# Optimization experiments

Hardware: AMD Instinct MI355X
Metric: run time of the kernel (lower is better)

## Reference

```python
import jax, jax.numpy as jnp
import numpy as np

N = 4096     # batch of positions
E = 32       # descriptor buckets (experts)
NBLK = 12    # residual blocks per head


def _ln(x, g, b, eps=1e-5):
    m = x.mean(-1, keepdims=True)
    v = ((x - m) ** 2).mean(-1, keepdims=True)
    return (x - m) / jnp.sqrt(v + eps) * g + b


def _gelu(x):
    return jax.nn.gelu(x, approximate=False)  # torch nn.GELU default = exact erf


def setup_inputs() -> dict:
    key = jax.random.key(0)
    ks = iter(jax.random.split(key, 64))

    def nrm(shape, scale=0.05):
        return jax.random.normal(next(ks), shape, jnp.float32) * scale

    return {
        "piece_idx": jax.random.randint(next(ks), (N, 64), 0, 12),
        "side_flag": jax.random.randint(next(ks), (N,), 0, 2),
        "ep_file": jax.random.randint(next(ks), (N,), 0, 8),
        "castle_ms": jax.random.uniform(next(ks), (N, 4), jnp.float32),
        "fifty_a": jax.random.uniform(next(ks), (N,), jnp.float32),
        "descriptor_index": jax.random.randint(next(ks), (N,), 0, E),
        # per-bucket embedding tables, stacked on a leading expert axis
        "Wp_w": nrm((E, 64, 12, 32)), "Wp_b": nrm((E, 64, 12, 32)),
        "Wc_w": nrm((E, 4, 32)), "Wc_b": nrm((E, 4, 32)),
        "Wep_w": nrm((E, 8, 32)), "Wep_b": nrm((E, 8, 32)),
        "Wf_w": nrm((E, 2, 32)), "Wf_b": nrm((E, 2, 32)),
        # per-bucket MLP head params (weights stored as [in,out])
        "fc1_w": nrm((E, 2240, 256)), "fc1_b": nrm((E, 256)),
        "ln1_g": jnp.ones((E, 256)), "ln1_b": jnp.zeros((E, 256)),
        "fc2_w": nrm((E, 256, 32)), "fc2_b": nrm((E, 32)),
        "ln2_g": jnp.ones((E, 32)), "ln2_b": jnp.zeros((E, 32)),
        "blkA_w": nrm((NBLK, E, 32, 32)), "blkA_b": nrm((NBLK, E, 32)),
        "blkA_g": jnp.ones((NBLK, E, 32)), "blkA_be": jnp.zeros((NBLK, E, 32)),
        "blkB_w": nrm((NBLK, E, 32, 32)), "blkB_b": nrm((NBLK, E, 32)),
        "blkB_g": jnp.ones((NBLK, E, 32)), "blkB_be": jnp.zeros((NBLK, E, 32)),
        "out_w": nrm((E, 32, 51)), "out_b": nrm((E, 51)),
        "bins": jnp.linspace(0.0, 1.0, 51),
    }


def reference(piece_idx, side_flag, ep_file, castle_ms, fifty_a, descriptor_index,
              Wp_w, Wp_b, Wc_w, Wc_b, Wep_w, Wep_b, Wf_w, Wf_b,
              fc1_w, fc1_b, ln1_g, ln1_b, fc2_w, fc2_b, ln2_g, ln2_b,
              blkA_w, blkA_b, blkA_g, blkA_be, blkB_w, blkB_b, blkB_g, blkB_be,
              out_w, out_b, bins):
    desc = descriptor_index
    side = side_flag.astype(bool)
    n = piece_idx.shape[0]

    # ---- per-bucket, side-selected embedding gathers -> x_emb [N,2240] ----
    sq = jnp.arange(64)
    pc = jnp.maximum(piece_idx, 0)                                 # clamp -1 -> 0
    w_emb = Wp_w[desc[:, None], sq[None, :], pc]                    # [N,64,32]
    b_emb = Wp_b[desc[:, None], sq[None, :], pc]
    piece_emb = jnp.where(side[:, None, None], b_emb, w_emb)
    piece_emb = piece_emb * (piece_idx >= 0)[..., None].astype(piece_emb.dtype)
    pieces_vec = piece_emb.reshape(n, 2048)

    Wc = jnp.where(side[:, None, None], Wc_b[desc], Wc_w[desc])     # [N,4,32]
    castle_vec = (castle_ms[..., None] * Wc).reshape(n, 128)

    Wep = jnp.where(side[:, None, None], Wep_b[desc], Wep_w[desc])  # [N,8,32]
    epc = jnp.maximum(ep_file, 0)
    ep_vec = jnp.take_along_axis(Wep, epc[:, None, None], axis=1)[:, 0]
    ep_vec = ep_vec * (ep_file >= 0)[:, None].astype(ep_vec.dtype)

    Wf = jnp.where(side[:, None, None], Wf_b[desc], Wf_w[desc])     # [N,2,32]
    fifty_vec = (1.0 - fifty_a)[:, None] * Wf[:, 0] + fifty_a[:, None] * Wf[:, 1]

    x = jnp.concatenate([pieces_vec, castle_vec, ep_vec, fifty_vec], axis=1)  # [N,2240]

    # ---- expert-routed dense layer: all-expert GEMM + per-token select ----
    def dense_moe(h, W, b):
        ha = jnp.einsum('nd,edh->neh', h, W)                        # [N,E,out]
        hsel = jnp.take_along_axis(ha, desc[:, None, None], axis=1)[:, 0]
        return hsel + b[desc]

    h = _ln(_gelu(dense_moe(x, fc1_w, fc1_b)), ln1_g[desc], ln1_b[desc])   # [N,256]
    h = _ln(_gelu(dense_moe(h, fc2_w, fc2_b)), ln2_g[desc], ln2_b[desc])   # [N,32]

    def blk(carry, p):
        wA, bA, gA, beA, wB, bB, gB, beB = p
        y = _ln(_gelu(dense_moe(carry, wA, bA)), gA[desc], beA[desc])
        y = _ln(_gelu(dense_moe(y, wB, bB)), gB[desc], beB[desc])
        return carry + y, None

    h, _ = jax.lax.scan(blk, h, (blkA_w, blkA_b, blkA_g, blkA_be,
                                 blkB_w, blkB_b, blkB_g, blkB_be))

    logits = dense_moe(_gelu(h), out_w, out_b)                      # [N,51]
    p_win = jnp.sum(jax.nn.softmax(logits, axis=-1) * bins, axis=-1, keepdims=True)
    return logits, p_win
```

## Files before the change

### kernel.cpp

```cpp
#include <hip/hip_runtime.h>
#include <math.h>

#define N 4096
#define E 32
#define NBLK 12
#define D_IN 2240
#define H1 256
#define H2 32
#define NOUT 51
#define MT 16
#define NPAD (N + E*(MT-1))
#define NTILE (NPAD/MT)
#define KSTEPS (D_IN/32)
#define KSPLIT 4
#define NROWS 4608
#define GMAX 96

typedef short s8v __attribute__((ext_vector_type(8)));
typedef float f4v __attribute__((ext_vector_type(4)));

__device__ __forceinline__ float gelu(float x){
    return 0.5f * x * (1.0f + erff(x * 0.70710678118654752f));
}
__device__ __forceinline__ unsigned short f2bf(float f){
    unsigned int u = __float_as_uint(f);
    unsigned int r = (u + 0x7fffu + ((u >> 16) & 1u)) >> 16;
    return (unsigned short)r;
}

__global__ void k_sort(const int* __restrict__ desc,
                       int* __restrict__ perm, int* __restrict__ tile_e,
                       int4* __restrict__ garr, int* __restrict__ ngroups){
    __shared__ int scnt[E];
    __shared__ int spoff[E+1];
    __shared__ int scur[E];
    int tid = threadIdx.x;
    if (tid < E) scnt[tid] = 0;
    __syncthreads();
    for (int n = tid; n < N; n += blockDim.x) atomicAdd(&scnt[desc[n]], 1);
    __syncthreads();
    if (tid == 0){
        int run = 0;
        for (int e = 0; e < E; e++){ spoff[e] = run; run += ((scnt[e] + MT - 1)/MT)*MT; }
        spoff[E] = run;
        int ng = 0;
        for (int e = 0; e < E; e++){
            int t0 = spoff[e]/MT, t1 = spoff[e+1]/MT;
            for (int t = t0; t < t1; t += 8){
                int nv = t1 - t; if (nv > 8) nv = 8;
                if (ng < GMAX) garr[ng] = make_int4(t, e, nv, 0);
                ng++;
            }
        }
        *ngroups = (ng > GMAX) ? GMAX : ng;
    }
    __syncthreads();
    if (tid < E) scur[tid] = spoff[tid];
    for (int p = tid; p < NPAD; p += blockDim.x) perm[p] = -1;
    __syncthreads();
    for (int n = tid; n < N; n += blockDim.x){
        int p = atomicAdd(&scur[desc[n]], 1);
        perm[p] = n;
    }
    for (int t = tid; t < NTILE; t += blockDim.x){
        int p0 = t*MT;
        int e = -1;
        if (p0 < spoff[E]){
            for (int q = 0; q < E; q++){
                if (p0 >= spoff[q] && p0 < spoff[q+1]){ e = q; break; }
            }
        }
        tile_e[t] = e;
    }
}

__global__ void k_convert(const float* __restrict__ W1, unsigned short* __restrict__ Wt){
    int kt = blockIdx.x;
    int nt = blockIdx.y;
    int e  = blockIdx.z;
    __shared__ float lds[64][65];
    int t = threadIdx.x;
    int k0 = kt*64, n0 = nt*64;
    int kk = t >> 4, nn = (t & 15) * 4;
    const float* src = W1 + ((size_t)e*D_IN + k0)*H1 + n0;
    #pragma unroll
    for (int r = 0; r < 4; r++){
        float4 v = *(const float4*)(src + (size_t)(kk + r*16)*H1 + nn);
        lds[kk + r*16][nn]   = v.x;
        lds[kk + r*16][nn+1] = v.y;
        lds[kk + r*16][nn+2] = v.z;
        lds[kk + r*16][nn+3] = v.w;
    }
    __syncthreads();
    int n = t >> 2, kq = t & 3;
    s8v p0, p1;
    #pragma unroll
    for (int j = 0; j < 8; j++) p0[j] = (short)f2bf(lds[kq*16 + j][n]);
    #pragma unroll
    for (int j = 0; j < 8; j++) p1[j] = (short)f2bf(lds[kq*16 + 8 + j][n]);
    unsigned short* dst = Wt + ((size_t)(e*H1 + n0 + n))*D_IN + k0 + kq*16;
    *(s8v*)dst       = p0;
    *(s8v*)(dst + 8) = p1;
}

__global__ void k_build(const int* __restrict__ perm,
                        const int* __restrict__ piece_idx,
                        const int* __restrict__ side_flag,
                        const int* __restrict__ ep_file,
                        const float* __restrict__ castle_ms,
                        const float* __restrict__ fifty_a,
                        const int* __restrict__ desc_idx,
                        const float* __restrict__ Wp_w, const float* __restrict__ Wp_b,
                        const float* __restrict__ Wc_w, const float* __restrict__ Wc_b,
                        const float* __restrict__ Wep_w, const float* __restrict__ Wep_b,
                        const float* __restrict__ Wf_w, const float* __restrict__ Wf_b,
                        unsigned short* __restrict__ xs){
    int pos = blockIdx.x;
    int row = perm[pos];
    unsigned short* xr = xs + (size_t)pos * D_IN;
    int tid = threadIdx.x;
    if (row < 0){
        s8v z = {0,0,0,0,0,0,0,0};
        for (int t = tid; t < D_IN/8; t += blockDim.x) *(s8v*)(xr + t*8) = z;
        return;
    }
    int d = desc_idx[row];
    int s = side_flag[row];
    __shared__ int pidx[64];
    if (tid < 64) pidx[tid] = piece_idx[row*64 + tid];
    __syncthreads();
    const float* Wp  = s ? Wp_b  : Wp_w;
    const float* Wc  = s ? Wc_b  : Wc_w;
    const float* Wep = s ? Wep_b : Wep_w;
    const float* Wf  = s ? Wf_b  : Wf_w;
    int ep  = ep_file[row];
    int epc = ep > 0 ? ep : 0;
    float a = fifty_a[row];
    for (int t = tid; t < D_IN/8; t += blockDim.x){
        int i0 = t*8;
        float v[8];
        if (i0 < 2048){
            int sq = i0 >> 5, c0 = i0 & 31;
            int pc = pidx[sq];
            float msk = pc >= 0 ? 1.0f : 0.0f;
            int pcc = pc > 0 ? pc : 0;
            const float* base = Wp + (((size_t)d*64 + sq)*12 + pcc)*32 + c0;
            float4 a0 = *(const float4*)base;
            float4 a1 = *(const float4*)(base + 4);
            v[0]=a0.x*msk; v[1]=a0.y*msk; v[2]=a0.z*msk; v[3]=a0.w*msk;
            v[4]=a1.x*msk; v[5]=a1.y*msk; v[6]=a1.z*msk; v[7]=a1.w*msk;
        } else if (i0 < 2176){
            int j = i0 - 2048; int ci = j >> 5, c0 = j & 31;
            float cv = castle_ms[row*4 + ci];
            const float* base = Wc + ((size_t)d*4 + ci)*32 + c0;
            float4 a0 = *(const float4*)base;
            float4 a1 = *(const float4*)(base + 4);
            v[0]=a0.x*cv; v[1]=a0.y*cv; v[2]=a0.z*cv; v[3]=a0.w*cv;
            v[4]=a1.x*cv; v[5]=a1.y*cv; v[6]=a1.z*cv; v[7]=a1.w*cv;
        } else if (i0 < 2208){
            int c0 = i0 - 2176;
            float msk = ep >= 0 ? 1.0f : 0.0f;
            const float* base = Wep + ((size_t)d*8 + epc)*32 + c0;
            float4 a0 = *(const float4*)base;
            float4 a1 = *(const float4*)(base + 4);
            v[0]=a0.x*msk; v[1]=a0.y*msk; v[2]=a0.z*msk; v[3]=a0.w*msk;
            v[4]=a1.x*msk; v[5]=a1.y*msk; v[6]=a1.z*msk; v[7]=a1.w*msk;
        } else {
            int c0 = i0 - 2208;
            #pragma unroll
            for (int j = 0; j < 8; j++)
                v[j] = (1.0f - a) * Wf[(size_t)d*64 + c0 + j] + a * Wf[(size_t)d*64 + 32 + c0 + j];
        }
        s8v p;
        #pragma unroll
        for (int j = 0; j < 8; j++) p[j] = (short)f2bf(v[j]);
        *(s8v*)(xr + i0) = p;
    }
}

__launch_bounds__(256)
__global__ void k_fc1(const int4* __restrict__ garr, const int* __restrict__ ngroups,
                      const unsigned short* __restrict__ xs,
                      const unsigned short* __restrict__ Wt,
                      float* __restrict__ h1p){
    int g = blockIdx.x;
    if (g >= *ngroups) return;
    int4 gi = garr[g];
    int tile0 = gi.x, e = gi.y, nv = gi.z;
    int kc = blockIdx.y, nh = blockIdx.z;
    int kstart = (kc <= 2) ? kc*18 : 53;
    int nsteps = (kc < 2) ? 18 : 17;
    int lane = threadIdx.x & 63, wave = threadIdx.x >> 6;
    int quad = lane >> 4, l16 = lane & 15;
    int col0 = nh*128 + wave*32 + l16;
    const unsigned short* Ab = xs + (size_t)(tile0*MT + l16)*D_IN + quad*8;
    const unsigned short* B0 = Wt + ((size_t)e*H1 + col0)*D_IN + quad*8;
    const unsigned short* B1 = B0 + (size_t)16*D_IN;
    f4v acc[8][2];
    #pragma unroll
    for (int mt = 0; mt < 8; mt++){ acc[mt][0] = (f4v){0.f,0.f,0.f,0.f}; acc[mt][1] = (f4v){0.f,0.f,0.f,0.f}; }
    int kend = kstart + nsteps;
    #pragma unroll 2
    for (int s = kstart; s < kend; s++){
        int ko = s*32;
        s8v b0 = *(const s8v*)(B0 + ko);
        s8v b1 = *(const s8v*)(B1 + ko);
        #pragma unroll
        for (int mt = 0; mt < 8; mt++){
            s8v av = *(const s8v*)(Ab + (size_t)mt*MT*D_IN + ko);
            acc[mt][0] = __builtin_amdgcn_mfma_f32_16x16x32_bf16(av, b0, acc[mt][0], 0, 0, 0);
            acc[mt][1] = __builtin_amdgcn_mfma_f32_16x16x32_bf16(av, b1, acc[mt][1], 0, 0, 0);
        }
    }
    float* out = h1p + (size_t)kc*NROWS*H1;
    #pragma unroll
    for (int mt = 0; mt < 8; mt++){
        if (mt >= nv) break;
        int posb = (tile0 + mt)*MT + quad*4;
        #pragma unroll
        for (int r = 0; r < 4; r++){
            out[(size_t)(posb + r)*H1 + col0]      = acc[mt][0][r];
            out[(size_t)(posb + r)*H1 + col0 + 16] = acc[mt][1][r];
        }
    }
}

__launch_bounds__(512)
__global__ void k_fc2(const int* __restrict__ tile_e,
                      const float* __restrict__ h1p,
                      const float* __restrict__ b1,
                      const float* __restrict__ g1, const float* __restrict__ be1,
                      const float* __restrict__ W2, const float* __restrict__ b2,
                      const float* __restrict__ g2, const float* __restrict__ be2,
                      float* __restrict__ h){
    int t = blockIdx.x;
    int e = tile_e[t];
    if (e < 0) return;
    __shared__ float sh[MT][H1+1];
    __shared__ float sW[H1*H2];
    __shared__ float sg[H1], sb[H1];
    int tid = threadIdx.x;
    const float4* Wsrc = (const float4*)(W2 + (size_t)e*H1*H2);
    for (int i = tid; i < H1*H2/4; i += 512) ((float4*)sW)[i] = Wsrc[i];
    if (tid < H1){ sg[tid] = g1[e*H1 + tid]; sb[tid] = be1[e*H1 + tid]; }
    for (int slot = tid; slot < MT*H1/4; slot += 512){
        int r = slot >> 6, c4 = (slot & 63) << 2;
        float4 sacc = {0.f,0.f,0.f,0.f};
        #pragma unroll
        for (int kc = 0; kc < KSPLIT; kc++){
            float4 v = *(const float4*)(h1p + ((size_t)kc*NROWS + t*MT + r)*H1 + c4);
            sacc.x += v.x; sacc.y += v.y; sacc.z += v.z; sacc.w += v.w;
        }
        float4 bb = *(const float4*)(b1 + e*H1 + c4);
        sh[r][c4]   = gelu(sacc.x + bb.x);
        sh[r][c4+1] = gelu(sacc.y + bb.y);
        sh[r][c4+2] = gelu(sacc.z + bb.z);
        sh[r][c4+3] = gelu(sacc.w + bb.w);
    }
    __syncthreads();
    int m = tid >> 5, c = tid & 31;
    float s = 0.f;
    for (int k = c; k < H1; k += 32) s += sh[m][k];
    for (int o = 16; o > 0; o >>= 1) s += __shfl_xor(s, o);
    float mean = s * (1.0f/H1);
    float v2 = 0.f;
    for (int k = c; k < H1; k += 32){ float d = sh[m][k] - mean; v2 += d*d; }
    for (int o = 16; o > 0; o >>= 1) v2 += __shfl_xor(v2, o);
    float rs = rsqrtf(v2 * (1.0f/H1) + 1e-5f);
    for (int k = c; k < H1; k += 32)
        sh[m][k] = (sh[m][k] - mean) * rs * sg[k] + sb[k];
    __syncthreads();
    float acc = b2[e*H2 + c];
    #pragma unroll 8
    for (int k = 0; k < H1; k++) acc = fmaf(sh[m][k], sW[k*H2 + c], acc);
    float y = gelu(acc);
    float ss = y;
    for (int o = 16; o > 0; o >>= 1) ss += __shfl_xor(ss, o);
    float mean2 = ss * (1.0f/H2);
    float dv = y - mean2;
    float vv = dv*dv;
    for (int o = 16; o > 0; o >>= 1) vv += __shfl_xor(vv, o);
    float var2 = vv * (1.0f/H2);
    float outv = dv * rsqrtf(var2 + 1e-5f) * g2[e*H2+c] + be2[e*H2+c];
    h[(size_t)(t*MT + m)*H2 + c] = outv;
}

__launch_bounds__(512)
__global__ void k_blocks(const int* __restrict__ tile_e,
                         const float* __restrict__ Aw, const float* __restrict__ Ab,
                         const float* __restrict__ Ag, const float* __restrict__ Abe,
                         const float* __restrict__ Bw, const float* __restrict__ Bb,
                         const float* __restrict__ Bg, const float* __restrict__ Bbe,
                         float* __restrict__ h){
    int t = blockIdx.x;
    int e = tile_e[t];
    if (e < 0) return;
    int m = threadIdx.x >> 5, c = threadIdx.x & 31;
    int pos = t*MT + m;
    float hv = h[(size_t)pos*H2 + c];
    __shared__ float sA[1024], sB[1024], shh[MT][33];
    for (int tb = 0; tb < NBLK; tb++){
        const float* A = Aw + ((size_t)tb*E + e)*1024;
        const float* B = Bw + ((size_t)tb*E + e)*1024;
        __syncthreads();
        for (int i = threadIdx.x; i < 1024; i += 512){ sA[i] = A[i]; sB[i] = B[i]; }
        shh[m][c] = hv;
        __syncthreads();
        float acc = Ab[((size_t)tb*E + e)*32 + c];
        #pragma unroll
        for (int k = 0; k < 32; k++) acc = fmaf(shh[m][k], sA[k*32 + c], acc);
        float y = gelu(acc);
        float s = y;
        for (int o = 16; o > 0; o >>= 1) s += __shfl_xor(s, o);
        float mean = s * (1.0f/32);
        float dv = y - mean;
        float v = dv*dv;
        for (int o = 16; o > 0; o >>= 1) v += __shfl_xor(v, o);
        float var = v * (1.0f/32);
        y = dv * rsqrtf(var + 1e-5f) * Ag[((size_t)tb*E+e)*32+c] + Abe[((size_t)tb*E+e)*32+c];
        __syncthreads();
        shh[m][c] = y;
        __syncthreads();
        acc = Bb[((size_t)tb*E + e)*32 + c];
        #pragma unroll
        for (int k = 0; k < 32; k++) acc = fmaf(shh[m][k], sB[k*32 + c], acc);
        y = gelu(acc);
        s = y;
        for (int o = 16; o > 0; o >>= 1) s += __shfl_xor(s, o);
        mean = s * (1.0f/32);
        dv = y - mean;
        v = dv*dv;
        for (int o = 16; o > 0; o >>= 1) v += __shfl_xor(v, o);
        var = v * (1.0f/32);
        y = dv * rsqrtf(var + 1e-5f) * Bg[((size_t)tb*E+e)*32+c] + Bbe[((size_t)tb*E+e)*32+c];
        hv += y;
    }
    h[(size_t)pos*H2 + c] = hv;
}

__global__ void k_out(const int* __restrict__ perm, const int* __restrict__ tile_e,
                      const float* __restrict__ h,
                      const float* __restrict__ Ow, const float* __restrict__ Ob,
                      const float* __restrict__ bins,
                      float* __restrict__ out){
    int wid = threadIdx.x >> 6, lane = threadIdx.x & 63;
    int pos = blockIdx.x*4 + wid;
    if (pos >= NPAD) return;
    int row = perm[pos];
    if (row < 0) return;
    int e = tile_e[pos / MT];
    float gv = 0.0f;
    if (lane < 32) gv = gelu(h[(size_t)pos*H2 + lane]);
    float acc = (lane < NOUT) ? Ob[e*NOUT + lane] : -INFINITY;
    const float* W = Ow + (size_t)e*32*NOUT;
    #pragma unroll
    for (int k = 0; k < 32; k++){
        float gk = __shfl(gv, k);
        if (lane < NOUT) acc = fmaf(gk, W[k*NOUT + lane], acc);
    }
    if (lane < NOUT) out[(size_t)row*NOUT + lane] = acc;
    float mx = acc;
    for (int o = 32; o > 0; o >>= 1) mx = fmaxf(mx, __shfl_xor(mx, o));
    float p = (lane < NOUT) ? expf(acc - mx) : 0.0f;
    float sum = p;
    for (int o = 32; o > 0; o >>= 1) sum += __shfl_xor(sum, o);
    float pb = (lane < NOUT) ? p * bins[lane] : 0.0f;
    float sb = pb;
    for (int o = 32; o > 0; o >>= 1) sb += __shfl_xor(sb, o);
    if (lane == 0) out[(size_t)N*NOUT + row] = sb / sum;
}

extern "C" void kernel_launch(void* const* d_in, const int* in_sizes, int n_in,
                              void* d_out, int out_size, void* d_ws, size_t ws_size,
                              hipStream_t stream){
    const int*   piece_idx = (const int*)d_in[0];
    const int*   side_flag = (const int*)d_in[1];
    const int*   ep_file   = (const int*)d_in[2];
    const float* castle_ms = (const float*)d_in[3];
    const float* fifty_a   = (const float*)d_in[4];
    const int*   desc      = (const int*)d_in[5];
    const float* Wp_w  = (const float*)d_in[6];
    const float* Wp_b  = (const float*)d_in[7];
    const float* Wc_w  = (const float*)d_in[8];
    const float* Wc_b  = (const float*)d_in[9];
    const float* Wep_w = (const float*)d_in[10];
    const float* Wep_b = (const float*)d_in[11];
    const float* Wf_w  = (const float*)d_in[12];
    const float* Wf_b  = (const float*)d_in[13];
    const float* fc1_w = (const float*)d_in[14];
    const float* fc1_b = (const float*)d_in[15];
    const float* ln1_g = (const float*)d_in[16];
    const float* ln1_b = (const float*)d_in[17];
    const float* fc2_w = (const float*)d_in[18];
    const float* fc2_b = (const float*)d_in[19];
    const float* ln2_g = (const float*)d_in[20];
    const float* ln2_b = (const float*)d_in[21];
    const float* blkA_w  = (const float*)d_in[22];
    const float* blkA_b  = (const float*)d_in[23];
    const float* blkA_g  = (const float*)d_in[24];
    const float* blkA_be = (const float*)d_in[25];
    const float* blkB_w  = (const float*)d_in[26];
    const float* blkB_b  = (const float*)d_in[27];
    const float* blkB_g  = (const float*)d_in[28];
    const float* blkB_be = (const float*)d_in[29];
    const float* out_w = (const float*)d_in[30];
    const float* out_b = (const float*)d_in[31];
    const float* bins  = (const float*)d_in[32];

    char* wsp = (char*)d_ws;
    auto alloc = [&](size_t bytes){ void* p = (void*)wsp; wsp += (bytes + 255) & ~(size_t)255; return p; };
    int*            perm    = (int*)            alloc((size_t)NPAD*4);
    int*            tile_e  = (int*)            alloc((size_t)NTILE*4);
    int4*           garr    = (int4*)           alloc((size_t)GMAX*16);
    int*            ngroups = (int*)            alloc(256);
    unsigned short* Wt      = (unsigned short*) alloc((size_t)E*H1*D_IN*2);
    unsigned short* xs      = (unsigned short*) alloc((size_t)(NPAD+128)*D_IN*2);
    float*          h1p     = (float*)          alloc((size_t)KSPLIT*NROWS*H1*4);
    float*          h       = (float*)          alloc((size_t)NPAD*H2*4);

    k_sort<<<1, 256, 0, stream>>>(desc, perm, tile_e, garr, ngroups);
    k_convert<<<dim3(D_IN/64, H1/64, E), 256, 0, stream>>>(fc1_w, Wt);
    k_build<<<NPAD, 256, 0, stream>>>(perm, piece_idx, side_flag, ep_file, castle_ms,
                                      fifty_a, desc, Wp_w, Wp_b, Wc_w, Wc_b,
                                      Wep_w, Wep_b, Wf_w, Wf_b, xs);
    k_fc1<<<dim3(GMAX, KSPLIT, 2), 256, 0, stream>>>(garr, ngroups, xs, Wt, h1p);
    k_fc2<<<NTILE, 512, 0, stream>>>(tile_e, h1p, fc1_b, ln1_g, ln1_b,
                                     fc2_w, fc2_b, ln2_g, ln2_b, h);
    k_blocks<<<NTILE, 512, 0, stream>>>(tile_e, blkA_w, blkA_b, blkA_g, blkA_be,
                                        blkB_w, blkB_b, blkB_g, blkB_be, h);
    k_out<<<(NPAD + 3)/4, 256, 0, stream>>>(perm, tile_e, h, out_w, out_b, bins, (float*)d_out);
}
```

Baseline: 330.4 us.

## Fuse fc2, residual blocks and output head into one wave-per-row tail kernel

Merges the fc2+LN, twelve residual blocks, and output/softmax kernels into a single kernel with one 64-lane wave per token row and 1024 threads per tile. The residual blocks now use wave shuffles and read weights directly from global memory instead of staging them in shared memory with block-wide barriers. The intermediate h buffer round-trip and two kernel launches go away. In exchange, each row's weight reads hit global/L2 repeatedly and the large 1024-thread blocks may reduce occupancy.

Result: slower. 374.9 us (+13.5%).

```diff
diff --git a/kernel.cpp b/kernel.cpp
--- a/kernel.cpp
+++ b/kernel.cpp
@@ -225,149 +225,158 @@
     }
 }
 
-__launch_bounds__(512)
-__global__ void k_fc2(const int* __restrict__ tile_e,
-                      const float* __restrict__ h1p,
-                      const float* __restrict__ b1,
-                      const float* __restrict__ g1, const float* __restrict__ be1,
-                      const float* __restrict__ W2, const float* __restrict__ b2,
-                      const float* __restrict__ g2, const float* __restrict__ be2,
-                      float* __restrict__ h){
+__launch_bounds__(1024)
+__global__ void k_tail(const int* __restrict__ tile_e, const int* __restrict__ perm,
+                       const float* __restrict__ h1p, const float* __restrict__ b1,
+                       const float* __restrict__ g1, const float* __restrict__ be1,
+                       const float* __restrict__ W2, const float* __restrict__ b2,
+                       const float* __restrict__ g2, const float* __restrict__ be2,
+                       const float* __restrict__ Aw, const float* __restrict__ Abv,
+                       const float* __restrict__ Ag, const float* __restrict__ Abe,
+                       const float* __restrict__ Bw, const float* __restrict__ Bb,
+                       const float* __restrict__ Bg, const float* __restrict__ Bbe,
+                       const float* __restrict__ Ow, const float* __restrict__ Ob,
+                       const float* __restrict__ bins,
+                       float* __restrict__ out){
     int t = blockIdx.x;
     int e = tile_e[t];
     if (e < 0) return;
-    __shared__ float sh[MT][H1+1];
+    int tid = threadIdx.x;
+    int wave = tid >> 6, lane = tid & 63;
+    int row = t*MT + wave;
+
     __shared__ float sW[H1*H2];
-    __shared__ float sg[H1], sb[H1];
-    int tid = threadIdx.x;
-    const float4* Wsrc = (const float4*)(W2 + (size_t)e*H1*H2);
-    for (int i = tid; i < H1*H2/4; i += 512) ((float4*)sW)[i] = Wsrc[i];
-    if (tid < H1){ sg[tid] = g1[e*H1 + tid]; sb[tid] = be1[e*H1 + tid]; }
-    for (int slot = tid; slot < MT*H1/4; slot += 512){
-        int r = slot >> 6, c4 = (slot & 63) << 2;
-        float4 sacc = {0.f,0.f,0.f,0.f};
-        #pragma unroll
-        for (int kc = 0; kc < KSPLIT; kc++){
-            float4 v = *(const float4*)(h1p + ((size_t)kc*NROWS + t*MT + r)*H1 + c4);
-            sacc.x += v.x; sacc.y += v.y; sacc.z += v.z; sacc.w += v.w;
-        }
-        float4 bb = *(const float4*)(b1 + e*H1 + c4);
-        sh[r][c4]   = gelu(sacc.x + bb.x);
-        sh[r][c4+1] = gelu(sacc.y + bb.y);
-        sh[r][c4+2] = gelu(sacc.z + bb.z);
-        sh[r][c4+3] = gelu(sacc.w + bb.w);
-    }
-    __syncthreads();
-    int m = tid >> 5, c = tid & 31;
-    float s = 0.f;
-    for (int k = c; k < H1; k += 32) s += sh[m][k];
-    for (int o = 16; o > 0; o >>= 1) s += __shfl_xor(s, o);
+    __shared__ float sh[MT][H1];
+    {
+        const float4* Wsrc = (const float4*)(W2 + (size_t)e*H1*H2);
+        ((float4*)sW)[tid]        = Wsrc[tid];
+        ((float4*)sW)[tid + 1024] = Wsrc[tid + 1024];
+    }
+    float4 v = {0.f,0.f,0.f,0.f};
+    #pragma unroll
+    for (int kc = 0; kc < KSPLIT; kc++){
+        float4 p = *(const float4*)(h1p + ((size_t)kc*NROWS + row)*H1 + lane*4);
+        v.x += p.x; v.y += p.y; v.z += p.z; v.w += p.w;
+    }
+    float4 bb = *(const float4*)(b1 + e*H1 + lane*4);
+    float a0 = gelu(v.x + bb.x), a1 = gelu(v.y + bb.y);
+    float a2 = gelu(v.z + bb.z), a3 = gelu(v.w + bb.w);
+    float s = a0 + a1 + a2 + a3;
+    #pragma unroll
+    for (int o = 32; o > 0; o >>= 1) s += __shfl_xor(s, o);
     float mean = s * (1.0f/H1);
-    float v2 = 0.f;
-    for (int k = c; k < H1; k += 32){ float d = sh[m][k] - mean; v2 += d*d; }
-    for (int o = 16; o > 0; o >>= 1) v2 += __shfl_xor(v2, o);
-    float rs = rsqrtf(v2 * (1.0f/H1) + 1e-5f);
-    for (int k = c; k < H1; k += 32)
-        sh[m][k] = (sh[m][k] - mean) * rs * sg[k] + sb[k];
-    __syncthreads();
-    float acc = b2[e*H2 + c];
+    float d0 = a0-mean, d1 = a1-mean, d2 = a2-mean, d3 = a3-mean;
+    float vr = d0*d0 + d1*d1 + d2*d2 + d3*d3;
+    #pragma unroll
+    for (int o = 32; o > 0; o >>= 1) vr += __shfl_xor(vr, o);
+    float rs = rsqrtf(vr * (1.0f/H1) + 1e-5f);
+    float4 gg = *(const float4*)(g1 + e*H1 + lane*4);
+    float4 gb = *(const float4*)(be1 + e*H1 + lane*4);
+    float4 hn;
+    hn.x = d0*rs*gg.x + gb.x; hn.y = d1*rs*gg.y + gb.y;
+    hn.z = d2*rs*gg.z + gb.z; hn.w = d3*rs*gg.w + gb.w;
+    *(float4*)(&sh[wave][lane*4]) = hn;
+    __syncthreads();
+
+    int c = lane & 31, kk = lane >> 5;
+    float ac0=0.f, ac1=0.f, ac2=0.f, ac3=0.f;
+    const float* shr = sh[wave];
     #pragma unroll 8
-    for (int k = 0; k < H1; k++) acc = fmaf(sh[m][k], sW[k*H2 + c], acc);
+    for (int j = 0; j < 128; j += 4){
+        int k = kk*128 + j;
+        ac0 = fmaf(shr[k],   sW[(k)*H2   + c], ac0);
+        ac1 = fmaf(shr[k+1], sW[(k+1)*H2 + c], ac1);
+        ac2 = fmaf(shr[k+2], sW[(k+2)*H2 + c], ac2);
+        ac3 = fmaf(shr[k+3], sW[(k+3)*H2 + c], ac3);
+    }
+    float acc = (ac0 + ac1) + (ac2 + ac3);
+    acc += __shfl_xor(acc, 32);
+    acc += b2[e*H2 + c];
     float y = gelu(acc);
     float ss = y;
+    #pragma unroll
     for (int o = 16; o > 0; o >>= 1) ss += __shfl_xor(ss, o);
     float mean2 = ss * (1.0f/H2);
     float dv = y - mean2;
     float vv = dv*dv;
+    #pragma unroll
     for (int o = 16; o > 0; o >>= 1) vv += __shfl_xor(vv, o);
-    float var2 = vv * (1.0f/H2);
-    float outv = dv * rsqrtf(var2 + 1e-5f) * g2[e*H2+c] + be2[e*H2+c];
-    h[(size_t)(t*MT + m)*H2 + c] = outv;
-}
-
-__launch_bounds__(512)
-__global__ void k_blocks(const int* __restrict__ tile_e,
-                         const float* __restrict__ Aw, const float* __restrict__ Ab,
-                         const float* __restrict__ Ag, const float* __restrict__ Abe,
-                         const float* __restrict__ Bw, const float* __restrict__ Bb,
-                         const float* __restrict__ Bg, const float* __restrict__ Bbe,
-                         float* __restrict__ h){
-    int t = blockIdx.x;
-    int e = tile_e[t];
-    if (e < 0) return;
-    int m = threadIdx.x >> 5, c = threadIdx.x & 31;
-    int pos = t*MT + m;
-    float hv = h[(size_t)pos*H2 + c];
-    __shared__ float sA[1024], sB[1024], shh[MT][33];
+    float hv = dv * rsqrtf(vv*(1.0f/H2) + 1e-5f) * g2[e*H2+c] + be2[e*H2+c];
+
+    #pragma unroll 1
     for (int tb = 0; tb < NBLK; tb++){
-        const float* A = Aw + ((size_t)tb*E + e)*1024;
-        const float* B = Bw + ((size_t)tb*E + e)*1024;
-        __syncthreads();
-        for (int i = threadIdx.x; i < 1024; i += 512){ sA[i] = A[i]; sB[i] = B[i]; }
-        shh[m][c] = hv;
-        __syncthreads();
-        float acc = Ab[((size_t)tb*E + e)*32 + c];
-        #pragma unroll
-        for (int k = 0; k < 32; k++) acc = fmaf(shh[m][k], sA[k*32 + c], acc);
-        float y = gelu(acc);
-        float s = y;
-        for (int o = 16; o > 0; o >>= 1) s += __shfl_xor(s, o);
-        float mean = s * (1.0f/32);
-        float dv = y - mean;
-        float v = dv*dv;
-        for (int o = 16; o > 0; o >>= 1) v += __shfl_xor(v, o);
-        float var = v * (1.0f/32);
-        y = dv * rsqrtf(var + 1e-5f) * Ag[((size_t)tb*E+e)*32+c] + Abe[((size_t)tb*E+e)*32+c];
-        __syncthreads();
-        shh[m][c] = y;
-        __syncthreads();
-        acc = Bb[((size_t)tb*E + e)*32 + c];
-        #pragma unroll
-        for (int k = 0; k < 32; k++) acc = fmaf(shh[m][k], sB[k*32 + c], acc);
-        y = gelu(acc);
-        s = y;
-        for (int o = 16; o > 0; o >>= 1) s += __shfl_xor(s, o);
-        mean = s * (1.0f/32);
-        dv = y - mean;
-        v = dv*dv;
-        for (int o = 16; o > 0; o >>= 1) v += __shfl_xor(v, o);
-        var = v * (1.0f/32);
-        y = dv * rsqrtf(var + 1e-5f) * Bg[((size_t)tb*E+e)*32+c] + Bbe[((size_t)tb*E+e)*32+c];
-        hv += y;
-    }
-    h[(size_t)pos*H2 + c] = hv;
-}
-
-__global__ void k_out(const int* __restrict__ perm, const int* __restrict__ tile_e,
-                      const float* __restrict__ h,
-                      const float* __restrict__ Ow, const float* __restrict__ Ob,
-                      const float* __restrict__ bins,
-                      float* __restrict__ out){
-    int wid = threadIdx.x >> 6, lane = threadIdx.x & 63;
-    int pos = blockIdx.x*4 + wid;
-    if (pos >= NPAD) return;
-    int row = perm[pos];
-    if (row < 0) return;
-    int e = tile_e[pos / MT];
-    float gv = 0.0f;
-    if (lane < 32) gv = gelu(h[(size_t)pos*H2 + lane]);
-    float acc = (lane < NOUT) ? Ob[e*NOUT + lane] : -INFINITY;
+        size_t wb = ((size_t)tb*E + e);
+        const float* A = Aw + wb*1024;
+        const float* B = Bw + wb*1024;
+        float b0=0.f,b1a=0.f,b2a=0.f,b3=0.f;
+        #pragma unroll
+        for (int j = 0; j < 16; j += 4){
+            int k = kk*16 + j;
+            b0  = fmaf(__shfl(hv, k),   A[(k)*32   + c], b0);
+            b1a = fmaf(__shfl(hv, k+1), A[(k+1)*32 + c], b1a);
+            b2a = fmaf(__shfl(hv, k+2), A[(k+2)*32 + c], b2a);
+            b3  = fmaf(__shfl(hv, k+3), A[(k+3)*32 + c], b3);
+        }
+        float ya = (b0 + b1a) + (b2a + b3);
+        ya += __shfl_xor(ya, 32);
+        ya += Abv[wb*32 + c];
+        ya = gelu(ya);
+        float sa = ya;
+        #pragma unroll
+        for (int o = 16; o > 0; o >>= 1) sa += __shfl_xor(sa, o);
+        float ma = sa * (1.0f/H2);
+        float da = ya - ma;
+        float va = da*da;
+        #pragma unroll
+        for (int o = 16; o > 0; o >>= 1) va += __shfl_xor(va, o);
+        float yA = da * rsqrtf(va*(1.0f/H2) + 1e-5f) * Ag[wb*32+c] + Abe[wb*32+c];
+        b0=0.f; b1a=0.f; b2a=0.f; b3=0.f;
+        #pragma unroll
+        for (int j = 0; j < 16; j += 4){
+            int k = kk*16 + j;
+            b0  = fmaf(__shfl(yA, k),   B[(k)*32   + c], b0);
+            b1a = fmaf(__shfl(yA, k+1), B[(k+1)*32 + c], b1a);
+            b2a = fmaf(__shfl(yA, k+2), B[(k+2)*32 + c], b2a);
+            b3  = fmaf(__shfl(yA, k+3), B[(k+3)*32 + c], b3);
+        }
+        float yb = (b0 + b1a) + (b2a + b3);
+        yb += __shfl_xor(yb, 32);
+        yb += Bb[wb*32 + c];
+        yb = gelu(yb);
+        float sb2 = yb;
+        #pragma unroll
+        for (int o = 16; o > 0; o >>= 1) sb2 += __shfl_xor(sb2, o);
+        float mb = sb2 * (1.0f/H2);
+        float db = yb - mb;
+        float vb = db*db;
+        #pragma unroll
+        for (int o = 16; o > 0; o >>= 1) vb += __shfl_xor(vb, o);
+        hv += db * rsqrtf(vb*(1.0f/H2) + 1e-5f) * Bg[wb*32+c] + Bbe[wb*32+c];
+    }
+
+    int orow = perm[row];
+    if (orow < 0) return;
+    float gv = gelu(hv);
+    float accl = (lane < NOUT) ? Ob[e*NOUT + lane] : -INFINITY;
     const float* W = Ow + (size_t)e*32*NOUT;
     #pragma unroll
     for (int k = 0; k < 32; k++){
         float gk = __shfl(gv, k);
-        if (lane < NOUT) acc = fmaf(gk, W[k*NOUT + lane], acc);
-    }
-    if (lane < NOUT) out[(size_t)row*NOUT + lane] = acc;
-    float mx = acc;
+        if (lane < NOUT) accl = fmaf(gk, W[k*NOUT + lane], accl);
+    }
+    if (lane < NOUT) out[(size_t)orow*NOUT + lane] = accl;
+    float mx = accl;
+    #pragma unroll
     for (int o = 32; o > 0; o >>= 1) mx = fmaxf(mx, __shfl_xor(mx, o));
-    float p = (lane < NOUT) ? expf(acc - mx) : 0.0f;
+    float p = (lane < NOUT) ? expf(accl - mx) : 0.0f;
     float sum = p;
+    #pragma unroll
     for (int o = 32; o > 0; o >>= 1) sum += __shfl_xor(sum, o);
     float pb = (lane < NOUT) ? p * bins[lane] : 0.0f;
     float sb = pb;
+    #pragma unroll
     for (int o = 32; o > 0; o >>= 1) sb += __shfl_xor(sb, o);
-    if (lane == 0) out[(size_t)N*NOUT + row] = sb / sum;
+    if (lane == 0) out[(size_t)N*NOUT + orow] = sb / sum;
 }
 
 extern "C" void kernel_launch(void* const* d_in, const int* in_sizes, int n_in,
@@ -416,7 +425,6 @@
     unsigned short* Wt      = (unsigned short*) alloc((size_t)E*H1*D_IN*2);
     unsigned short* xs      = (unsigned short*) alloc((size_t)(NPAD+128)*D_IN*2);
     float*          h1p     = (float*)          alloc((size_t)KSPLIT*NROWS*H1*4);
-    float*          h       = (float*)          alloc((size_t)NPAD*H2*4);
 
     k_sort<<<1, 256, 0, stream>>>(desc, perm, tile_e, garr, ngroups);
     k_convert<<<dim3(D_IN/64, H1/64, E), 256, 0, stream>>>(fc1_w, Wt);
@@ -424,9 +432,9 @@
                                       fifty_a, desc, Wp_w, Wp_b, Wc_w, Wc_b,
                                       Wep_w, Wep_b, Wf_w, Wf_b, xs);
     k_fc1<<<dim3(GMAX, KSPLIT, 2), 256, 0, stream>>>(garr, ngroups, xs, Wt, h1p);
-    k_fc2<<<NTILE, 512, 0, stream>>>(tile_e, h1p, fc1_b, ln1_g, ln1_b,
-                                     fc2_w, fc2_b, ln2_g, ln2_b, h);
-    k_blocks<<<NTILE, 512, 0, stream>>>(tile_e, blkA_w, blkA_b, blkA_g, blkA_be,
-                                        blkB_w, blkB_b, blkB_g, blkB_be, h);
-    k_out<<<(NPAD + 3)/4, 256, 0, stream>>>(perm, tile_e, h, out_w, out_b, bins, (float*)d_out);
-}
+    k_tail<<<NTILE, 1024, 0, stream>>>(tile_e, perm, h1p, fc1_b, ln1_g, ln1_b,
+                                       fc2_w, fc2_b, ln2_g, ln2_b,
+                                       blkA_w, blkA_b, blkA_g, blkA_be,
+                                       blkB_w, blkB_b, blkB_g, blkB_be,
+                                       out_w, out_b, bins, (float*)d_out);
+}
```
